# Kernel tuning notes

Measured on AMD Instinct MI355X. Metric: run time of the kernel, lower is better.

Reference implementation:

```python
import jax, jax.numpy as jnp
import numpy as np

N_NODES = 50000
N_EDGES = 800000
D_IN = 64
D_RADIAL = 128


def setup_inputs() -> dict:
    key = jax.random.key(0)
    k1, k2, k3, k4, k5 = jax.random.split(key, 5)
    x = jax.random.normal(k1, (N_NODES, D_IN), dtype=jnp.float32)
    edge_basis = jax.random.normal(k2, (N_EDGES, D_RADIAL), dtype=jnp.float32)
    src = jax.random.randint(k3, (N_EDGES,), 0, N_NODES, dtype=jnp.int32)
    dst = jax.random.randint(k4, (N_EDGES,), 0, N_NODES, dtype=jnp.int32)
    # kaiming normal fan_in, linear nonlinearity: std = 1/sqrt(fan_in)
    W = jax.random.normal(k5, (D_IN, D_RADIAL), dtype=jnp.float32) / jnp.sqrt(
        jnp.float32(D_RADIAL))
    b = jnp.zeros((D_IN,), dtype=jnp.float32)
    return {"x": x, "edge_basis": edge_basis, "src": src, "dst": dst,
            "W": W, "b": b}


def reference(x, edge_basis, src, dst, W, b):
    # per-edge radial filter: Linear(d_radial -> d_in)  [E, d_in]
    filt = jnp.einsum('er,dr->ed', edge_basis, W) + b
    # gather source node features, multiply by filter  [E, d_in]
    m = x[src] * filt
    # scatter-sum messages into destination nodes      [N, d_in]
    h = jax.ops.segment_sum(m, dst, num_segments=x.shape[0])
    return h
```

## Files before the change

### kernel.cpp

```cpp
#include <hip/hip_runtime.h>

#define N_NODES  50000
#define N_EDGES  800000
#define D_IN     64
#define D_RADIAL 128
#define NTILES   (N_EDGES / 64)

typedef __bf16 bf16x8 __attribute__((ext_vector_type(8)));
typedef float  f32x4  __attribute__((ext_vector_type(4)));
typedef short  s16x8  __attribute__((ext_vector_type(8)));

__device__ inline unsigned int pack_bf16_pair(float lo, float hi) {
    return __builtin_amdgcn_perm(__float_as_uint(hi), __float_as_uint(lo), 0x07060302u);
}

__device__ inline short f2bf_rne(float f) {
    unsigned int u = __float_as_uint(f);
    u += 0x7FFFu + ((u >> 16) & 1u);
    return (short)(u >> 16);
}

__global__ __launch_bounds__(256) void edge_msg_kernel(
    const float* __restrict__ x,
    const float* __restrict__ eb,
    const int*   __restrict__ src,
    const int*   __restrict__ dst,
    const float* __restrict__ W,
    const float* __restrict__ bias_p,
    float*       __restrict__ out)
{
    const int lane = threadIdx.x & 63;
    const int wv   = threadIdx.x >> 6;
    const int l15  = lane & 15;
    const int quad = lane >> 4;

    bf16x8 wfrag[4][4];
    #pragma unroll
    for (int nt = 0; nt < 4; ++nt) {
        const int d = nt * 16 + l15;
        #pragma unroll
        for (int kt = 0; kt < 4; ++kt) {
            const float* p = W + d * D_RADIAL + kt * 32 + quad * 8;
            s16x8 s;
            #pragma unroll
            for (int j = 0; j < 8; ++j) s[j] = f2bf_rne(p[j]);
            wfrag[nt][kt] = __builtin_bit_cast(bf16x8, s);
        }
    }
    float bv[4];
    #pragma unroll
    for (int nt = 0; nt < 4; ++nt) bv[nt] = bias_p[nt * 16 + l15];

    for (int tile = blockIdx.x; tile < NTILES; tile += gridDim.x) {
        const int ebase = tile * 64 + wv * 16;

        f32x4 acc[4];
        #pragma unroll
        for (int nt = 0; nt < 4; ++nt) acc[nt] = (f32x4){0.f, 0.f, 0.f, 0.f};

        #pragma unroll
        for (int kt = 0; kt < 4; ++kt) {
            const float* p = eb + (long)(ebase + l15) * D_RADIAL + kt * 32 + quad * 8;
            f32x4 a0 = *(const f32x4*)(p);
            f32x4 a1 = *(const f32x4*)(p + 4);
            int4 packed;
            packed.x = pack_bf16_pair(a0[0], a0[1]);
            packed.y = pack_bf16_pair(a0[2], a0[3]);
            packed.z = pack_bf16_pair(a1[0], a1[1]);
            packed.w = pack_bf16_pair(a1[2], a1[3]);
            bf16x8 afrag = __builtin_bit_cast(bf16x8, packed);
            #pragma unroll
            for (int nt = 0; nt < 4; ++nt)
                acc[nt] = __builtin_amdgcn_mfma_f32_16x16x32_bf16(
                    afrag, wfrag[nt][kt], acc[nt], 0, 0, 0);
        }

        const int erow = ebase + quad * 4;
        #pragma unroll
        for (int reg = 0; reg < 4; ++reg) {
            const int e  = erow + reg;
            const int sv = src[e];
            const int dv = dst[e];
            const float* xrow = x   + (long)sv * D_IN;
            float*       orow = out + (long)dv * D_IN;
            #pragma unroll
            for (int nt = 0; nt < 4; ++nt) {
                const int d = nt * 16 + l15;
                const float val = (acc[nt][reg] + bv[nt]) * xrow[d];
                unsafeAtomicAdd(orow + d, val);
            }
        }
    }
}

extern "C" void kernel_launch(void* const* d_in, const int* in_sizes, int n_in,
                              void* d_out, int out_size, void* d_ws, size_t ws_size,
                              hipStream_t stream) {
    const float* x    = (const float*)d_in[0];
    const float* eb   = (const float*)d_in[1];
    const int*   src  = (const int*)d_in[2];
    const int*   dst  = (const int*)d_in[3];
    const float* W    = (const float*)d_in[4];
    const float* bias = (const float*)d_in[5];
    float* out = (float*)d_out;

    hipMemsetAsync(d_out, 0, (size_t)N_NODES * D_IN * sizeof(float), stream);

    edge_msg_kernel<<<1024, 256, 0, stream>>>(x, eb, src, dst, W, bias, out);
}
```

Measured before the change: 714.8 us.

## Replace atomic scatter with CSR sort-by-destination and segmented gather reduction

Builds a destination-sorted layout each call: histogram of dst, prefix scan, and per-edge rank via atomic slot claiming. The message kernel writes bf16 messages to their sorted slot, and a gather kernel sums each node's contiguous segment without float atomics. This removes 51M float atomics in exchange for several extra launches, integer atomics, and a 100MB bf16 message buffer round trip, and it rounds messages to bf16 before summation, which costs precision. The new path runs only if the workspace is large enough.

New measurement: 697.5 us. 2.4% less time.

```diff
diff --git a/kernel.cpp b/kernel.cpp
--- a/kernel.cpp
+++ b/kernel.cpp
@@ -14,10 +14,184 @@
     return __builtin_amdgcn_perm(__float_as_uint(hi), __float_as_uint(lo), 0x07060302u);
 }
 
-__device__ inline short f2bf_rne(float f) {
+__device__ inline unsigned short f2bf_rne(float f) {
     unsigned int u = __float_as_uint(f);
     u += 0x7FFFu + ((u >> 16) & 1u);
-    return (short)(u >> 16);
+    return (unsigned short)(u >> 16);
+}
+
+constexpr size_t ws_align(size_t x) { return (x + 255) & ~(size_t)255; }
+constexpr size_t WS_CNT  = 0;
+constexpr size_t WS_OFF  = ws_align(WS_CNT  + (size_t)N_NODES * 4);
+constexpr size_t WS_CUR  = ws_align(WS_OFF  + (size_t)(N_NODES + 1) * 4);
+constexpr size_t WS_BSUM = ws_align(WS_CUR  + (size_t)N_NODES * 4);
+constexpr size_t WS_RANK = ws_align(WS_BSUM + 512);
+constexpr size_t WS_MSG  = ws_align(WS_RANK + (size_t)N_EDGES * 4);
+constexpr size_t WS_REQUIRED = WS_MSG + (size_t)N_EDGES * D_IN * 2;
+
+#define SCAN_B    512
+#define SCAN_NBLK ((N_NODES + SCAN_B - 1) / SCAN_B)
+static_assert(SCAN_NBLK <= 128, "scan_tops assumes <=128 blocks");
+
+__global__ __launch_bounds__(256) void hist_kernel(const int* __restrict__ dst,
+                                                   int* __restrict__ cnt) {
+    int i = blockIdx.x * 256 + threadIdx.x;
+    if (i < N_EDGES) atomicAdd(&cnt[dst[i]], 1);
+}
+
+__global__ __launch_bounds__(SCAN_B) void scan_block(const int* __restrict__ cnt,
+                                                     int* __restrict__ offs,
+                                                     int* __restrict__ bsum) {
+    const int t = threadIdx.x, b = blockIdx.x;
+    const int i = b * SCAN_B + t;
+    int v = (i < N_NODES) ? cnt[i] : 0;
+    __shared__ int s[SCAN_B];
+    s[t] = v;
+    __syncthreads();
+    for (int o = 1; o < SCAN_B; o <<= 1) {
+        int add = (t >= o) ? s[t - o] : 0;
+        __syncthreads();
+        s[t] += add;
+        __syncthreads();
+    }
+    if (i < N_NODES) offs[i] = s[t];
+    if (t == SCAN_B - 1) bsum[b] = s[t];
+}
+
+__global__ __launch_bounds__(128) void scan_tops(int* __restrict__ bsum) {
+    const int t = threadIdx.x;
+    __shared__ int s[128];
+    int v = (t < SCAN_NBLK) ? bsum[t] : 0;
+    s[t] = v;
+    __syncthreads();
+    for (int o = 1; o < 128; o <<= 1) {
+        int add = (t >= o) ? s[t - o] : 0;
+        __syncthreads();
+        s[t] += add;
+        __syncthreads();
+    }
+    if (t < SCAN_NBLK) bsum[t] = s[t] - v;
+}
+
+__global__ __launch_bounds__(SCAN_B) void finalize_off(const int* __restrict__ cnt,
+                                                       int* __restrict__ offs,
+                                                       const int* __restrict__ bsum,
+                                                       int* __restrict__ cur) {
+    const int i = blockIdx.x * SCAN_B + threadIdx.x;
+    if (i < N_NODES) {
+        int e = offs[i] - cnt[i] + bsum[blockIdx.x];
+        offs[i] = e;
+        cur[i]  = e;
+    }
+    if (i == 0) offs[N_NODES] = N_EDGES;
+}
+
+__global__ __launch_bounds__(256) void scatter_rank(const int* __restrict__ dst,
+                                                    int* __restrict__ cur,
+                                                    int* __restrict__ rank) {
+    int i = blockIdx.x * 256 + threadIdx.x;
+    if (i < N_EDGES) rank[i] = atomicAdd(&cur[dst[i]], 1);
+}
+
+__global__ __launch_bounds__(256) void msg_kernel(
+    const float* __restrict__ x,
+    const float* __restrict__ eb,
+    const int*   __restrict__ src,
+    const int*   __restrict__ rank,
+    const float* __restrict__ W,
+    const float* __restrict__ bias_p,
+    unsigned short* __restrict__ msg)
+{
+    const int lane = threadIdx.x & 63;
+    const int wv   = threadIdx.x >> 6;
+    const int l15  = lane & 15;
+    const int quad = lane >> 4;
+
+    bf16x8 wfrag[4][4];
+    #pragma unroll
+    for (int nt = 0; nt < 4; ++nt) {
+        const int d = nt * 16 + l15;
+        #pragma unroll
+        for (int kt = 0; kt < 4; ++kt) {
+            const float* p = W + d * D_RADIAL + kt * 32 + quad * 8;
+            s16x8 s;
+            #pragma unroll
+            for (int j = 0; j < 8; ++j) s[j] = (short)f2bf_rne(p[j]);
+            wfrag[nt][kt] = __builtin_bit_cast(bf16x8, s);
+        }
+    }
+    float bv[4];
+    #pragma unroll
+    for (int nt = 0; nt < 4; ++nt) bv[nt] = bias_p[nt * 16 + l15];
+
+    for (int tile = blockIdx.x; tile < NTILES; tile += gridDim.x) {
+        const int ebase = tile * 64 + wv * 16;
+        const int erow  = ebase + quad * 4;
+
+        int sv[4], rk[4];
+        #pragma unroll
+        for (int reg = 0; reg < 4; ++reg) {
+            sv[reg] = src[erow + reg];
+            rk[reg] = rank[erow + reg];
+        }
+
+        f32x4 acc[4];
+        #pragma unroll
+        for (int nt = 0; nt < 4; ++nt) acc[nt] = (f32x4){0.f, 0.f, 0.f, 0.f};
+
+        #pragma unroll
+        for (int kt = 0; kt < 4; ++kt) {
+            const float* p = eb + (long)(ebase + l15) * D_RADIAL + kt * 32 + quad * 8;
+            f32x4 a0 = *(const f32x4*)(p);
+            f32x4 a1 = *(const f32x4*)(p + 4);
+            int4 packed;
+            packed.x = pack_bf16_pair(a0[0], a0[1]);
+            packed.y = pack_bf16_pair(a0[2], a0[3]);
+            packed.z = pack_bf16_pair(a1[0], a1[1]);
+            packed.w = pack_bf16_pair(a1[2], a1[3]);
+            bf16x8 afrag = __builtin_bit_cast(bf16x8, packed);
+            #pragma unroll
+            for (int nt = 0; nt < 4; ++nt)
+                acc[nt] = __builtin_amdgcn_mfma_f32_16x16x32_bf16(
+                    afrag, wfrag[nt][kt], acc[nt], 0, 0, 0);
+        }
+
+        #pragma unroll
+        for (int reg = 0; reg < 4; ++reg) {
+            const float*    xrow = x   + (long)sv[reg] * D_IN;
+            unsigned short* mrow = msg + (long)rk[reg] * D_IN;
+            #pragma unroll
+            for (int nt = 0; nt < 4; ++nt) {
+                const int d = nt * 16 + l15;
+                mrow[d] = f2bf_rne((acc[nt][reg] + bv[nt]) * xrow[d]);
+            }
+        }
+    }
+}
+
+__global__ __launch_bounds__(256) void gather_out(
+    const unsigned short* __restrict__ msg,
+    const int* __restrict__ offs,
+    float* __restrict__ out)
+{
+    const int lane = threadIdx.x & 63;
+    const int wid  = blockIdx.x * 4 + (threadIdx.x >> 6);
+    const int wstr = gridDim.x * 4;
+    for (int n = wid; n < N_NODES; n += wstr) {
+        const int j0 = offs[n], j1 = offs[n + 1];
+        const unsigned short* p = msg + (size_t)j0 * D_IN + lane;
+        float a0 = 0.f, a1 = 0.f, a2 = 0.f, a3 = 0.f;
+        int j = j0;
+        for (; j + 4 <= j1; j += 4, p += 4 * D_IN) {
+            a0 += __uint_as_float((unsigned int)p[0]        << 16);
+            a1 += __uint_as_float((unsigned int)p[D_IN]     << 16);
+            a2 += __uint_as_float((unsigned int)p[2 * D_IN] << 16);
+            a3 += __uint_as_float((unsigned int)p[3 * D_IN] << 16);
+        }
+        for (; j < j1; ++j, p += D_IN)
+            a0 += __uint_as_float((unsigned int)p[0] << 16);
+        out[(size_t)n * D_IN + lane] = (a0 + a1) + (a2 + a3);
+    }
 }
 
 __global__ __launch_bounds__(256) void edge_msg_kernel(
@@ -43,7 +217,7 @@
             const float* p = W + d * D_RADIAL + kt * 32 + quad * 8;
             s16x8 s;
             #pragma unroll
-            for (int j = 0; j < 8; ++j) s[j] = f2bf_rne(p[j]);
+            for (int j = 0; j < 8; ++j) s[j] = (short)f2bf_rne(p[j]);
             wfrag[nt][kt] = __builtin_bit_cast(bf16x8, s);
         }
     }
@@ -104,7 +278,25 @@
     const float* bias = (const float*)d_in[5];
     float* out = (float*)d_out;
 
-    hipMemsetAsync(d_out, 0, (size_t)N_NODES * D_IN * sizeof(float), stream);
-
-    edge_msg_kernel<<<1024, 256, 0, stream>>>(x, eb, src, dst, W, bias, out);
-}
+    if (ws_size >= WS_REQUIRED) {
+        char* ws   = (char*)d_ws;
+        int*  cnt  = (int*)(ws + WS_CNT);
+        int*  offs = (int*)(ws + WS_OFF);
+        int*  cur  = (int*)(ws + WS_CUR);
+        int*  bsum = (int*)(ws + WS_BSUM);
+        int*  rank = (int*)(ws + WS_RANK);
+        unsigned short* msg = (unsigned short*)(ws + WS_MSG);
+
+        hipMemsetAsync(cnt, 0, (size_t)N_NODES * 4, stream);
+        hist_kernel  <<<(N_EDGES + 255) / 256, 256, 0, stream>>>(dst, cnt);
+        scan_block   <<<SCAN_NBLK, SCAN_B, 0, stream>>>(cnt, offs, bsum);
+        scan_tops    <<<1, 128, 0, stream>>>(bsum);
+        finalize_off <<<SCAN_NBLK, SCAN_B, 0, stream>>>(cnt, offs, bsum, cur);
+        scatter_rank <<<(N_EDGES + 255) / 256, 256, 0, stream>>>(dst, cur, rank);
+        msg_kernel   <<<1280, 256, 0, stream>>>(x, eb, src, rank, W, bias, msg);
+        gather_out   <<<1024, 256, 0, stream>>>(msg, offs, out);
+    } else {
+        hipMemsetAsync(d_out, 0, (size_t)N_NODES * D_IN * sizeof(float), stream);
+        edge_msg_kernel<<<1024, 256, 0, stream>>>(x, eb, src, dst, W, bias, out);
+    }
+}
```
